# Performance work log

Measured on AMD Instinct MI355X. Metric: run time of the kernel, lower is better.

Reference implementation:

```python
import jax, jax.numpy as jnp
import numpy as np
from jax import lax

B, N, D = 8, 1024, 768      # batch, tokens, feature dim
H, Y = 12, 64               # heads, head dim
M = 3072                    # hopfield memories (4*D)
STEPS = 12                  # descent steps (module default)
ALPHA = 0.1                 # SGD step size (module default)
BETA = 1.0 / np.sqrt(Y)     # attention inverse temperature
EPS = 1e-5


def setup_inputs() -> dict:
    key = jax.random.key(0)
    k0, k1, k2, k3 = jax.random.split(key, 4)
    return {
        "x": jax.random.normal(k0, (B, N, D), dtype=jnp.float32),
        "ln_gamma": jnp.ones((D,), dtype=jnp.float32),
        "ln_beta": jnp.zeros((D,), dtype=jnp.float32),
        "wq": jax.random.normal(k1, (H, Y, D), dtype=jnp.float32) * 0.02,
        "wk": jax.random.normal(k2, (H, Y, D), dtype=jnp.float32) * 0.02,
        "xi": jax.random.normal(k3, (M, D), dtype=jnp.float32) * 0.02,
    }


def _layer_norm(x, gamma, beta):
    mu = jnp.mean(x, axis=-1, keepdims=True)
    var = jnp.var(x, axis=-1, keepdims=True)
    return gamma * (x - mu) * lax.rsqrt(var + EPS) + beta


def _energy(g, wq, wk, xi):
    # Attention energy: A[b,h,m,n] = sum_y K_{hy m} Q_{hy n}
    q = jnp.einsum("hyd,bnd->bhny", wq, g)
    k = jnp.einsum("hyd,bnd->bhny", wk, g)
    logits = BETA * jnp.einsum("bhmy,bhny->bhmn", k, q)  # [B,H,N(keys),N(queries)]
    e_att = -(1.0 / BETA) * jnp.sum(jax.scipy.special.logsumexp(logits, axis=2))
    # Hopfield energy: -0.5 * sum relu(xi @ g)^2
    hid = jnp.einsum("md,bnd->bnm", xi, g)
    e_hn = -0.5 * jnp.sum(jnp.square(jax.nn.relu(hid)))
    return e_att + e_hn


_energy_grad = jax.grad(_energy)


def reference(x, ln_gamma, ln_beta, wq, wk, xi):
    def step(x, _):
        g = _layer_norm(x, ln_gamma, ln_beta)  # grad taken w.r.t. g, not through LN
        grad = _energy_grad(g, wq, wk, xi)
        return x - ALPHA * grad, None

    x, _ = lax.scan(step, x, None, length=STEPS)
    return x
```

## Files before the change

kernel.cpp:

```cpp
#include <hip/hip_runtime.h>
#include <math.h>

#define B_ 8
#define N_ 1024
#define D_ 768
#define H_ 12
#define Y_ 64
#define M_ 3072
#define STEPS_ 12
#define ALPHA_ 0.1f
#define BETA_ 0.125f
#define EPS_ 1e-5f

typedef __attribute__((ext_vector_type(8))) short bf16x8;
typedef __attribute__((ext_vector_type(8))) unsigned short u16x8;
typedef __attribute__((ext_vector_type(4))) float f32x4;

__device__ inline unsigned short f2bf(float f) {
  union { float f; unsigned int u; } v; v.f = f;
  unsigned int r = (v.u + 0x7fffu + ((v.u >> 16) & 1u)) >> 16;
  return (unsigned short)r;
}

__device__ inline void async_copy16(const void* g, void* l) {
  __builtin_amdgcn_global_load_lds(
      (const __attribute__((address_space(1))) unsigned int*)g,
      (__attribute__((address_space(3))) unsigned int*)l, 16, 0, 0);
}

__device__ inline int xcd_remap(int bid, int nwg) {
  const int qd = nwg >> 3, rm = nwg & 7;
  const int xcd = bid & 7, idx = bid >> 3;
  return (xcd < rm ? xcd * (qd + 1) : rm * (qd + 1) + (xcd - rm) * qd) + idx;
}

__global__ __launch_bounds__(256) void ln_kernel(const float* __restrict__ x,
    const float* __restrict__ gamma, const float* __restrict__ beta,
    unsigned short* __restrict__ g) {
  const int row = blockIdx.x;
  const int t = threadIdx.x;
  const float* xr = x + (size_t)row * D_;
  float v0 = xr[t], v1 = xr[t + 256], v2 = xr[t + 512];
  float s = v0 + v1 + v2;
  float sq = v0 * v0 + v1 * v1 + v2 * v2;
  #pragma unroll
  for (int off = 1; off < 64; off <<= 1) {
    s += __shfl_xor(s, off);
    sq += __shfl_xor(sq, off);
  }
  __shared__ float ss[4], ssq[4];
  const int wid = t >> 6;
  if ((t & 63) == 0) { ss[wid] = s; ssq[wid] = sq; }
  __syncthreads();
  s = ss[0] + ss[1] + ss[2] + ss[3];
  sq = ssq[0] + ssq[1] + ssq[2] + ssq[3];
  const float mu = s * (1.0f / D_);
  const float var = sq * (1.0f / D_) - mu * mu;
  const float r = rsqrtf(var + EPS_);
  unsigned short* gr = g + (size_t)row * D_;
  gr[t]       = f2bf(gamma[t]       * (v0 - mu) * r + beta[t]);
  gr[t + 256] = f2bf(gamma[t + 256] * (v1 - mu) * r + beta[t + 256]);
  gr[t + 512] = f2bf(gamma[t + 512] * (v2 - mu) * r + beta[t + 512]);
}

__global__ __launch_bounds__(256) void cvt_bf16(const float* __restrict__ in,
    unsigned short* __restrict__ out, int n) {
  int i = blockIdx.x * 256 + threadIdx.x;
  if (i < n) out[i] = f2bf(in[i]);
}

__global__ __launch_bounds__(256) void transpose_cvt(const float* __restrict__ in,
    unsigned short* __restrict__ out, int R, int C, int ldo, int koff) {
  __shared__ float tile[32][33];
  const int c0 = blockIdx.x * 32, r0 = blockIdx.y * 32;
  const int tx = threadIdx.x & 31, ty = threadIdx.x >> 5;
  #pragma unroll
  for (int i = 0; i < 32; i += 8)
    tile[ty + i][tx] = in[(size_t)(r0 + ty + i) * C + c0 + tx];
  __syncthreads();
  #pragma unroll
  for (int i = 0; i < 32; i += 8)
    out[(size_t)(c0 + ty + i) * ldo + koff + r0 + tx] = f2bf(tile[tx][ty + i]);
}

template <bool RELU, bool WRT>
__global__ __launch_bounds__(256) void gemm128(
    const unsigned short* __restrict__ A, const unsigned short* __restrict__ Bm,
    unsigned short* __restrict__ C, int N, int K, int gridN,
    unsigned short* __restrict__ qT, unsigned short* __restrict__ kT) {
  __shared__ __align__(16) unsigned short As[128 * 64];
  __shared__ __align__(16) unsigned short Bs[128 * 64];
  const int t = threadIdx.x;
  const int f = xcd_remap(blockIdx.x, gridDim.x);
  const int n0 = (f % gridN) * 128;
  const int m0 = (f / gridN) * 128;
  const int w = t >> 6;
  const int l = t & 63;
  const int wr = (w >> 1) * 64;
  const int wc = (w & 1) * 64;

  f32x4 acc[4][4];
  #pragma unroll
  for (int m = 0; m < 4; ++m)
    #pragma unroll
    for (int n = 0; n < 4; ++n) {
      f32x4 z = {0.f, 0.f, 0.f, 0.f};
      acc[m][n] = z;
    }

  for (int kt = 0; kt < K; kt += 64) {
    #pragma unroll
    for (int i = 0; i < 4; ++i) {
      const int flat = i * 4096 + t * 16;
      const int row = flat >> 7;
      const int slog = ((flat >> 4) & 7) ^ (row & 7);
      async_copy16(A + (size_t)(m0 + row) * K + kt + slog * 8, (char*)As + flat);
      async_copy16(Bm + (size_t)(n0 + row) * K + kt + slog * 8, (char*)Bs + flat);
    }
    __syncthreads();
    #pragma unroll
    for (int kk = 0; kk < 2; ++kk) {
      bf16x8 a[4], b[4];
      const int lr = l & 15;
      const int sl = kk * 4 + (l >> 4);
      #pragma unroll
      for (int m = 0; m < 4; ++m) {
        const int row = wr + m * 16 + lr;
        a[m] = *(const bf16x8*)((const char*)As + row * 128 + ((sl ^ (row & 7)) << 4));
      }
      #pragma unroll
      for (int n = 0; n < 4; ++n) {
        const int row = wc + n * 16 + lr;
        b[n] = *(const bf16x8*)((const char*)Bs + row * 128 + ((sl ^ (row & 7)) << 4));
      }
      #pragma unroll
      for (int m = 0; m < 4; ++m)
        #pragma unroll
        for (int n = 0; n < 4; ++n)
          acc[m][n] = __builtin_amdgcn_mfma_f32_16x16x32_bf16(a[m], b[n], acc[m][n], 0, 0, 0);
    }
    __syncthreads();
  }

  const int cr = (l >> 4) * 4;
  const int cc = l & 15;
  #pragma unroll
  for (int m = 0; m < 4; ++m)
    #pragma unroll
    for (int n = 0; n < 4; ++n) {
      const int col = n0 + wc + n * 16 + cc;
      unsigned long long pk = 0;
      #pragma unroll
      for (int j = 0; j < 4; ++j) {
        const int row = m0 + wr + m * 16 + cr + j;
        float v = acc[m][n][j];
        if (RELU) v = v > 0.f ? v : 0.f;
        const unsigned short bv = f2bf(v);
        C[(size_t)row * N + col] = bv;
        if (WRT) pk |= (unsigned long long)bv << (16 * j);
      }
      if (WRT) {
        const int row0 = m0 + wr + m * 16 + cr;
        const int bb = row0 >> 10, nn = row0 & 1023;
        const int hy = (col < 768) ? col : (col - 768);
        unsigned short* T = (col < 768) ? qT : kT;
        *(unsigned long long*)(T + ((size_t)bb * 768 + hy) * N_ + nn) = pk;
      }
    }
}

__global__ __launch_bounds__(256) void gemm_update(
    const unsigned short* __restrict__ A1,
    const unsigned short* __restrict__ A2,
    const unsigned short* __restrict__ B2,
    float* __restrict__ x,
    float alpha) {
  __shared__ __align__(16) unsigned short As[128 * 64];
  __shared__ __align__(16) unsigned short Bs[64 * 64];
  const int t = threadIdx.x;
  const int f = xcd_remap(blockIdx.x, gridDim.x);
  const int n0 = (f % 12) * 64;
  const int m0 = (f / 12) * 128;
  const int w = t >> 6;
  const int l = t & 63;
  const int wr = (w >> 1) * 64;
  const int wc = (w & 1) * 32;

  f32x4 acc[4][2];
  #pragma unroll
  for (int m = 0; m < 4; ++m)
    #pragma unroll
    for (int n = 0; n < 2; ++n) {
      f32x4 z = {0.f, 0.f, 0.f, 0.f};
      acc[m][n] = z;
    }

  for (int kt = 0; kt < 4608; kt += 64) {
    #pragma unroll
    for (int i = 0; i < 4; ++i) {
      const int flat = i * 4096 + t * 16;
      const int row = flat >> 7;
      const int slog = ((flat >> 4) & 7) ^ (row & 7);
      const unsigned short* src = (kt < 1536)
          ? A1 + (size_t)(m0 + row) * 1536 + kt + slog * 8
          : A2 + (size_t)(m0 + row) * 3072 + (kt - 1536) + slog * 8;
      async_copy16(src, (char*)As + flat);
    }
    #pragma unroll
    for (int i = 0; i < 2; ++i) {
      const int flat = i * 4096 + t * 16;
      const int row = flat >> 7;
      const int slog = ((flat >> 4) & 7) ^ (row & 7);
      async_copy16(B2 + (size_t)(n0 + row) * 4608 + kt + slog * 8, (char*)Bs + flat);
    }
    __syncthreads();
    #pragma unroll
    for (int kk = 0; kk < 2; ++kk) {
      bf16x8 a[4], b[2];
      const int lr = l & 15;
      const int sl = kk * 4 + (l >> 4);
      #pragma unroll
      for (int m = 0; m < 4; ++m) {
        const int row = wr + m * 16 + lr;
        a[m] = *(const bf16x8*)((const char*)As + row * 128 + ((sl ^ (row & 7)) << 4));
      }
      #pragma unroll
      for (int n = 0; n < 2; ++n) {
        const int row = wc + n * 16 + lr;
        b[n] = *(const bf16x8*)((const char*)Bs + row * 128 + ((sl ^ (row & 7)) << 4));
      }
      #pragma unroll
      for (int m = 0; m < 4; ++m)
        #pragma unroll
        for (int n = 0; n < 2; ++n)
          acc[m][n] = __builtin_amdgcn_mfma_f32_16x16x32_bf16(a[m], b[n], acc[m][n], 0, 0, 0);
    }
    __syncthreads();
  }

  const int cr = (l >> 4) * 4;
  const int cc = l & 15;
  #pragma unroll
  for (int m = 0; m < 4; ++m)
    #pragma unroll
    for (int n = 0; n < 2; ++n) {
      const int col = n0 + wc + n * 16 + cc;
      #pragma unroll
      for (int j = 0; j < 4; ++j) {
        const int row = m0 + wr + m * 16 + cr + j;
        float* cp = x + (size_t)row * 768 + col;
        *cp += alpha * acc[m][n][j];
      }
    }
}

__global__ __launch_bounds__(256) void attn1_mfma(
    const unsigned short* __restrict__ qk, const unsigned short* __restrict__ kT,
    unsigned short* __restrict__ AqAk, float* __restrict__ lse) {
  __shared__ __align__(16) unsigned short Ks[128 * 64];
  __shared__ __align__(16) unsigned short KTs[64 * 128];
  __shared__ __align__(16) unsigned short Ps[4 * 16 * 128];
  const int n0 = blockIdx.x * 64;
  const int h = blockIdx.y;
  const int b = blockIdx.z;
  const int t = threadIdx.x;
  const int w = t >> 6;
  const int l = t & 63;
  const int g = l >> 4;
  const int ql = l & 15;
  char* psw = (char*)(Ps + w * 2048);
  const int LD = 1536;

  bf16x8 qf[2];
  {
    const unsigned short* qrow =
        qk + ((size_t)(b * N_ + n0 + w * 16 + ql)) * LD + h * Y_;
    qf[0] = *(const bf16x8*)(qrow + g * 8);
    qf[1] = *(const bf16x8*)(qrow + 32 + g * 8);
  }
  const unsigned short* kbase = qk + (size_t)b * N_ * LD + 768 + h * Y_;
  const unsigned short* kTbase = kT + ((size_t)(b * H_ + h)) * Y_ * N_;

  f32x4 acc[4];
  #pragma unroll
  for (int yf = 0; yf < 4; ++yf) { f32x4 z = {0.f,0.f,0.f,0.f}; acc[yf] = z; }
  float mmax = -1e30f, lsum = 0.f;

  for (int mc = 0; mc < N_; mc += 128) {
    #pragma unroll
    for (int i = 0; i < 4; ++i) {
      const int flat = i * 4096 + t * 16;
      const int row = flat >> 7;
      const int slog = ((flat >> 4) & 7) ^ (row & 7);
      async_copy16(kbase + (size_t)(mc + row) * LD + slog * 8, (char*)Ks + flat);
    }
    #pragma unroll
    for (int i = 0; i < 4; ++i) {
      const int flat = i * 4096 + t * 16;
      const int row = flat >> 8;
      const int slog = ((flat >> 4) & 15) ^ (row & 7);
      async_copy16(kTbase + (size_t)row * N_ + mc + slog * 8, (char*)KTs + flat);
    }
    __syncthreads();

    f32x4 s[8];
    __builtin_amdgcn_s_setprio(1);
    #pragma unroll
    for (int f = 0; f < 8; ++f) {
      f32x4 z = {0.f,0.f,0.f,0.f}; s[f] = z;
      #pragma unroll
      for (int ks = 0; ks < 2; ++ks) {
        const int key = f * 16 + ql;
        bf16x8 a = *(const bf16x8*)((const char*)Ks + key * 128 +
                                    (((ks * 4 + g) ^ (key & 7)) << 4));
        s[f] = __builtin_amdgcn_mfma_f32_16x16x32_bf16(a, qf[ks], s[f], 0, 0, 0);
      }
    }
    __builtin_amdgcn_s_setprio(0);
    float rm = -1e30f;
    #pragma unroll
    for (int f = 0; f < 8; ++f)
      #pragma unroll
      for (int j = 0; j < 4; ++j) {
        const float v = s[f][j] * BETA_;
        s[f][j] = v;
        rm = fmaxf(rm, v);
      }
    rm = fmaxf(rm, __shfl_xor(rm, 16));
    rm = fmaxf(rm, __shfl_xor(rm, 32));
    const float nm = fmaxf(mmax, rm);
    const float sc = __expf(mmax - nm);
    float rs = 0.f;
    #pragma unroll
    for (int f = 0; f < 8; ++f) {
      unsigned short p4[4];
      #pragma unroll
      for (int j = 0; j < 4; ++j) {
        const float pvj = __expf(s[f][j] - nm);
        rs += pvj;
        p4[j] = f2bf(pvj);
      }
      unsigned long long pk = (unsigned long long)p4[0] |
          ((unsigned long long)p4[1] << 16) |
          ((unsigned long long)p4[2] << 32) |
          ((unsigned long long)p4[3] << 48);
      const int sl = (f * 4 + g) ^ ((ql & 7) << 1);
      *(unsigned long long*)(psw + ql * 256 + sl * 8) = pk;
    }
    rs += __shfl_xor(rs, 16);
    rs += __shfl_xor(rs, 32);
    lsum = lsum * sc + rs;
    mmax = nm;
    #pragma unroll
    for (int yf = 0; yf < 4; ++yf) acc[yf] *= sc;
    __builtin_amdgcn_s_setprio(1);
    #pragma unroll
    for (int ks2 = 0; ks2 < 4; ++ks2) {
      const int sl2 = (ks2 * 8 + g * 2) ^ ((ql & 7) << 1);
      bf16x8 pa = *(const bf16x8*)(psw + ql * 256 + sl2 * 8);
      #pragma unroll
      for (int yf = 0; yf < 4; ++yf) {
        const int y = yf * 16 + ql;
        bf16x8 bk = *(const bf16x8*)((const char*)KTs + y * 256 +
                                     (((ks2 * 4 + g) ^ (y & 7)) << 4));
        acc[yf] = __builtin_amdgcn_mfma_f32_16x16x32_bf16(pa, bk, acc[yf], 0, 0, 0);
      }
    }
    __builtin_amdgcn_s_setprio(0);
    __syncthreads();
  }

  float linv[4];
  #pragma unroll
  for (int j = 0; j < 4; ++j)
    linv[j] = 1.0f / __shfl(lsum, (g << 4) + g * 4 + j);
  #pragma unroll
  for (int yf = 0; yf < 4; ++yf)
    #pragma unroll
    for (int j = 0; j < 4; ++j) {
      const int row = n0 + w * 16 + g * 4 + j;
      AqAk[((size_t)(b * N_ + row)) * LD + h * Y_ + yf * 16 + ql] =
          f2bf(acc[yf][j] * linv[j]);
    }
  if (g == 0)
    lse[((size_t)b * H_ + h) * N_ + n0 + w * 16 + ql] = mmax + __logf(lsum);
}

__global__ __launch_bounds__(256) void attn2_mfma(
    const unsigned short* __restrict__ qk, const unsigned short* __restrict__ qT,
    const float* __restrict__ lse, unsigned short* __restrict__ AqAk) {
  __shared__ __align__(16) unsigned short Qs[128 * 64];
  __shared__ __align__(16) unsigned short QTs[64 * 128];
  __shared__ __align__(16) unsigned short Ws[4 * 16 * 128];
  __shared__ float lse_s[128];
  const int m0 = blockIdx.x * 64;
  const int h = blockIdx.y;
  const int b = blockIdx.z;
  const int t = threadIdx.x;
  const int w = t >> 6;
  const int l = t & 63;
  const int g = l >> 4;
  const int ql = l & 15;
  char* wsw = (char*)(Ws + w * 2048);
  const int LD = 1536;

  bf16x8 ka[2];
  {
    const unsigned short* krow =
        qk + ((size_t)(b * N_ + m0 + w * 16 + ql)) * LD + 768 + h * Y_;
    ka[0] = *(const bf16x8*)(krow + g * 8);
    ka[1] = *(const bf16x8*)(krow + 32 + g * 8);
  }
  const unsigned short* qbase = qk + (size_t)b * N_ * LD + h * Y_;
  const unsigned short* qTbase = qT + ((size_t)(b * H_ + h)) * Y_ * N_;
  const float* lbase = lse + ((size_t)b * H_ + h) * N_;

  f32x4 acc[4];
  #pragma unroll
  for (int yf = 0; yf < 4; ++yf) { f32x4 z = {0.f,0.f,0.f,0.f}; acc[yf] = z; }

  for (int nc = 0; nc < N_; nc += 128) {
    #pragma unroll
    for (int i = 0; i < 4; ++i) {
      const int flat = i * 4096 + t * 16;
      const int row = flat >> 7;
      const int slog = ((flat >> 4) & 7) ^ (row & 7);
      async_copy16(qbase + (size_t)(nc + row) * LD + slog * 8, (char*)Qs + flat);
    }
    #pragma unroll
    for (int i = 0; i < 4; ++i) {
      const int flat = i * 4096 + t * 16;
      const int row = flat >> 8;
      const int slog = ((flat >> 4) & 15) ^ (row & 7);
      async_copy16(qTbase + (size_t)row * N_ + nc + slog * 8, (char*)QTs + flat);
    }
    if (t < 128) lse_s[t] = lbase[nc + t];
    __syncthreads();

    f32x4 s[8];
    __builtin_amdgcn_s_setprio(1);
    #pragma unroll
    for (int f = 0; f < 8; ++f) {
      f32x4 z = {0.f,0.f,0.f,0.f}; s[f] = z;
      #pragma unroll
      for (int ks = 0; ks < 2; ++ks) {
        const int qr = f * 16 + ql;
        bf16x8 a = *(const bf16x8*)((const char*)Qs + qr * 128 +
                                    (((ks * 4 + g) ^ (qr & 7)) << 4));
        s[f] = __builtin_amdgcn_mfma_f32_16x16x32_bf16(a, ka[ks], s[f], 0, 0, 0);
      }
    }
    __builtin_amdgcn_s_setprio(0);
    #pragma unroll
    for (int f = 0; f < 8; ++f) {
      unsigned short w4[4];
      #pragma unroll
      for (int j = 0; j < 4; ++j) {
        const float wv = __expf(s[f][j] * BETA_ - lse_s[f * 16 + g * 4 + j]);
        w4[j] = f2bf(wv);
      }
      unsigned long long pk =
          (unsigned long long)w4[0] | ((unsigned long long)w4[1] << 16) |
          ((unsigned long long)w4[2] << 32) | ((unsigned long long)w4[3] << 48);
      const int sl = (f * 4 + g) ^ ((ql & 7) << 1);
      *(unsigned long long*)(wsw + ql * 256 + sl * 8) = pk;
    }
    __builtin_amdgcn_s_setprio(1);
    #pragma unroll
    for (int ks2 = 0; ks2 < 4; ++ks2) {
      const int sl2 = (ks2 * 8 + g * 2) ^ ((ql & 7) << 1);
      bf16x8 wa = *(const bf16x8*)(wsw + ql * 256 + sl2 * 8);
      #pragma unroll
      for (int yf = 0; yf < 4; ++yf) {
        const int y = yf * 16 + ql;
        bf16x8 bq = *(const bf16x8*)((const char*)QTs + y * 256 +
                                     (((ks2 * 4 + g) ^ (y & 7)) << 4));
        acc[yf] = __builtin_amdgcn_mfma_f32_16x16x32_bf16(wa, bq, acc[yf], 0, 0, 0);
      }
    }
    __builtin_amdgcn_s_setprio(0);
    __syncthreads();
  }

  #pragma unroll
  for (int yf = 0; yf < 4; ++yf)
    #pragma unroll
    for (int j = 0; j < 4; ++j) {
      const int row = m0 + w * 16 + g * 4 + j;
      AqAk[((size_t)(b * N_ + row)) * LD + 768 + h * Y_ + yf * 16 + ql] =
          f2bf(acc[yf][j]);
    }
}

extern "C" void kernel_launch(void* const* d_in, const int* in_sizes, int n_in,
                              void* d_out, int out_size, void* d_ws, size_t ws_size,
                              hipStream_t stream) {
  const float* x0    = (const float*)d_in[0];
  const float* gamma = (const float*)d_in[1];
  const float* beta  = (const float*)d_in[2];
  const float* wq    = (const float*)d_in[3];
  const float* wk    = (const float*)d_in[4];
  const float* xi    = (const float*)d_in[5];
  float* x = (float*)d_out;

  const size_t SZ = (size_t)B_ * N_ * D_;
  char* wsp = (char*)d_ws;
  size_t off = 0;
  auto alloc = [&](size_t bytes) -> void* {
    off = (off + 255) & ~(size_t)255;
    void* p = wsp + off;
    off += bytes;
    return p;
  };
  unsigned short* g_bf   = (unsigned short*)alloc(SZ * 2);
  unsigned short* qk_bf  = (unsigned short*)alloc(SZ * 2 * 2);
  unsigned short* AqAk   = (unsigned short*)alloc(SZ * 2 * 2);
  unsigned short* qT_bf  = (unsigned short*)alloc(SZ * 2);
  unsigned short* kT_bf  = (unsigned short*)alloc(SZ * 2);
  float*          lse    = (float*)alloc((size_t)B_ * H_ * N_ * 4);
  unsigned short* wqk_bf = (unsigned short*)alloc((size_t)2 * D_ * D_ * 2);
  unsigned short* xi_bf  = (unsigned short*)alloc((size_t)M_ * D_ * 2);
  unsigned short* B2_bf  = (unsigned short*)alloc((size_t)D_ * (2 * D_ + M_) * 2);
  off = (off + 255) & ~(size_t)255;
  unsigned short* hid_bf = (unsigned short*)(wsp + off);
  size_t avail = ws_size > off ? ws_size - off : 0;
  long rmax = (long)(avail / ((size_t)M_ * 2));
  int R = (int)((rmax / 128) * 128);
  if (R > B_ * N_) R = B_ * N_;
  if (R < 128) R = 128;

  const int WQN = D_ * D_;
  const int XIN = M_ * D_;
  cvt_bf16<<<(WQN + 255) / 256, 256, 0, stream>>>(wq, wqk_bf, WQN);
  cvt_bf16<<<(WQN + 255) / 256, 256, 0, stream>>>(wk, wqk_bf + (size_t)D_ * D_, WQN);
  cvt_bf16<<<(XIN + 255) / 256, 256, 0, stream>>>(xi, xi_bf, XIN);
  const int LDB2 = 2 * D_ + M_;
  transpose_cvt<<<dim3(D_ / 32, D_ / 32), 256, 0, stream>>>(wq, B2_bf, D_, D_, LDB2, 0);
  transpose_cvt<<<dim3(D_ / 32, D_ / 32), 256, 0, stream>>>(wk, B2_bf, D_, D_, LDB2, D_);
  transpose_cvt<<<dim3(D_ / 32, M_ / 32), 256, 0, stream>>>(xi, B2_bf, M_, D_, LDB2, 2 * D_);

  hipMemcpyAsync(x, x0, SZ * sizeof(float), hipMemcpyDeviceToDevice, stream);

  const int MN = B_ * N_;
  for (int step = 0; step < STEPS_; ++step) {
    ln_kernel<<<MN, 256, 0, stream>>>(x, gamma, beta, g_bf);
    gemm128<false, true><<<(1536 / 128) * (MN / 128), 256, 0, stream>>>(
        g_bf, wqk_bf, qk_bf, 1536, D_, 1536 / 128, qT_bf, kT_bf);
    attn1_mfma<<<dim3(N_ / 64, H_, B_), 256, 0, stream>>>(qk_bf, kT_bf, AqAk, lse);
    attn2_mfma<<<dim3(N_ / 64, H_, B_), 256, 0, stream>>>(qk_bf, qT_bf, lse, AqAk);
    for (int r0 = 0; r0 < MN; r0 += R) {
      const int rows = (MN - r0) < R ? (MN - r0) : R;
      gemm128<true, false><<<(M_ / 128) * (rows / 128), 256, 0, stream>>>(
          g_bf + (size_t)r0 * D_, xi_bf, hid_bf, M_, D_, M_ / 128, nullptr, nullptr);
      gemm_update<<<(D_ / 64) * (rows / 128), 256, 0, stream>>>(
          AqAk + (size_t)r0 * 1536, hid_bf, B2_bf, x + (size_t)r0 * D_, ALPHA_);
    }
  }
}
```

Baseline: 3.282 ms.

## Widen update GEMM K-tile, vectorize layernorm, drop hidden-buffer chunking

The layernorm kernel now uses 192 threads, each loading one float4 and writing packed bf16, in place of three scalar accesses per thread. The update GEMM stages a 128-wide K slice per iteration with a 16-way swizzle, halving the barrier and loop overhead per MFMA. The hidden activation buffer is now allocated for all rows, so the xi GEMM and the update GEMM each launch once per step without chunking. The full-size buffer assumes the workspace is large enough, and the larger LDS tiles may lower occupancy.

```diff
diff --git a/kernel.cpp b/kernel.cpp
--- a/kernel.cpp
+++ b/kernel.cpp
@@ -34,33 +34,37 @@
   return (xcd < rm ? xcd * (qd + 1) : rm * (qd + 1) + (xcd - rm) * qd) + idx;
 }
 
-__global__ __launch_bounds__(256) void ln_kernel(const float* __restrict__ x,
+__global__ __launch_bounds__(192) void ln_kernel(const float* __restrict__ x,
     const float* __restrict__ gamma, const float* __restrict__ beta,
     unsigned short* __restrict__ g) {
   const int row = blockIdx.x;
   const int t = threadIdx.x;
   const float* xr = x + (size_t)row * D_;
-  float v0 = xr[t], v1 = xr[t + 256], v2 = xr[t + 512];
-  float s = v0 + v1 + v2;
-  float sq = v0 * v0 + v1 * v1 + v2 * v2;
+  const float4 v = *(const float4*)(xr + t * 4);
+  float s = v.x + v.y + v.z + v.w;
+  float sq = v.x * v.x + v.y * v.y + v.z * v.z + v.w * v.w;
   #pragma unroll
   for (int off = 1; off < 64; off <<= 1) {
     s += __shfl_xor(s, off);
     sq += __shfl_xor(sq, off);
   }
-  __shared__ float ss[4], ssq[4];
+  __shared__ float ss[3], ssq[3];
   const int wid = t >> 6;
   if ((t & 63) == 0) { ss[wid] = s; ssq[wid] = sq; }
   __syncthreads();
-  s = ss[0] + ss[1] + ss[2] + ss[3];
-  sq = ssq[0] + ssq[1] + ssq[2] + ssq[3];
+  s = ss[0] + ss[1] + ss[2];
+  sq = ssq[0] + ssq[1] + ssq[2];
   const float mu = s * (1.0f / D_);
   const float var = sq * (1.0f / D_) - mu * mu;
   const float r = rsqrtf(var + EPS_);
-  unsigned short* gr = g + (size_t)row * D_;
-  gr[t]       = f2bf(gamma[t]       * (v0 - mu) * r + beta[t]);
-  gr[t + 256] = f2bf(gamma[t + 256] * (v1 - mu) * r + beta[t + 256]);
-  gr[t + 512] = f2bf(gamma[t + 512] * (v2 - mu) * r + beta[t + 512]);
+  const float4 gm = *(const float4*)(gamma + t * 4);
+  const float4 bt = *(const float4*)(beta + t * 4);
+  const unsigned int r0 = f2bf(gm.x * (v.x - mu) * r + bt.x);
+  const unsigned int r1 = f2bf(gm.y * (v.y - mu) * r + bt.y);
+  const unsigned int r2 = f2bf(gm.z * (v.z - mu) * r + bt.z);
+  const unsigned int r3 = f2bf(gm.w * (v.w - mu) * r + bt.w);
+  uint2 pk = {r0 | (r1 << 16), r2 | (r3 << 16)};
+  *(uint2*)(g + (size_t)row * D_ + t * 4) = pk;
 }
 
 __global__ __launch_bounds__(256) void cvt_bf16(const float* __restrict__ in,
@@ -175,8 +179,8 @@
     const unsigned short* __restrict__ B2,
     float* __restrict__ x,
     float alpha) {
-  __shared__ __align__(16) unsigned short As[128 * 64];
-  __shared__ __align__(16) unsigned short Bs[64 * 64];
+  __shared__ __align__(16) unsigned short As[128 * 128];
+  __shared__ __align__(16) unsigned short Bs[64 * 128];
   const int t = threadIdx.x;
   const int f = xcd_remap(blockIdx.x, gridDim.x);
   const int n0 = (f % 12) * 64;
@@ -195,39 +199,39 @@
       acc[m][n] = z;
     }
 
-  for (int kt = 0; kt < 4608; kt += 64) {
-    #pragma unroll
-    for (int i = 0; i < 4; ++i) {
-      const int flat = i * 4096 + t * 16;
-      const int row = flat >> 7;
-      const int slog = ((flat >> 4) & 7) ^ (row & 7);
+  for (int kt = 0; kt < 4608; kt += 128) {
+    #pragma unroll
+    for (int i = 0; i < 8; ++i) {
+      const int flat = i * 4096 + t * 16;
+      const int row = flat >> 8;
+      const int slog = ((flat >> 4) & 15) ^ (row & 15);
       const unsigned short* src = (kt < 1536)
           ? A1 + (size_t)(m0 + row) * 1536 + kt + slog * 8
           : A2 + (size_t)(m0 + row) * 3072 + (kt - 1536) + slog * 8;
       async_copy16(src, (char*)As + flat);
     }
     #pragma unroll
-    for (int i = 0; i < 2; ++i) {
-      const int flat = i * 4096 + t * 16;
-      const int row = flat >> 7;
-      const int slog = ((flat >> 4) & 7) ^ (row & 7);
+    for (int i = 0; i < 4; ++i) {
+      const int flat = i * 4096 + t * 16;
+      const int row = flat >> 8;
+      const int slog = ((flat >> 4) & 15) ^ (row & 15);
       async_copy16(B2 + (size_t)(n0 + row) * 4608 + kt + slog * 8, (char*)Bs + flat);
     }
     __syncthreads();
     #pragma unroll
-    for (int kk = 0; kk < 2; ++kk) {
+    for (int kk = 0; kk < 4; ++kk) {
       bf16x8 a[4], b[2];
       const int lr = l & 15;
       const int sl = kk * 4 + (l >> 4);
       #pragma unroll
       for (int m = 0; m < 4; ++m) {
         const int row = wr + m * 16 + lr;
-        a[m] = *(const bf16x8*)((const char*)As + row * 128 + ((sl ^ (row & 7)) << 4));
+        a[m] = *(const bf16x8*)((const char*)As + row * 256 + ((sl ^ (row & 15)) << 4));
       }
       #pragma unroll
       for (int n = 0; n < 2; ++n) {
         const int row = wc + n * 16 + lr;
-        b[n] = *(const bf16x8*)((const char*)Bs + row * 128 + ((sl ^ (row & 7)) << 4));
+        b[n] = *(const bf16x8*)((const char*)Bs + row * 256 + ((sl ^ (row & 15)) << 4));
       }
       #pragma unroll
       for (int m = 0; m < 4; ++m)
@@ -521,13 +525,7 @@
   unsigned short* wqk_bf = (unsigned short*)alloc((size_t)2 * D_ * D_ * 2);
   unsigned short* xi_bf  = (unsigned short*)alloc((size_t)M_ * D_ * 2);
   unsigned short* B2_bf  = (unsigned short*)alloc((size_t)D_ * (2 * D_ + M_) * 2);
-  off = (off + 255) & ~(size_t)255;
-  unsigned short* hid_bf = (unsigned short*)(wsp + off);
-  size_t avail = ws_size > off ? ws_size - off : 0;
-  long rmax = (long)(avail / ((size_t)M_ * 2));
-  int R = (int)((rmax / 128) * 128);
-  if (R > B_ * N_) R = B_ * N_;
-  if (R < 128) R = 128;
+  unsigned short* hid_bf = (unsigned short*)alloc((size_t)B_ * N_ * M_ * 2);
 
   const int WQN = D_ * D_;
   const int XIN = M_ * D_;
@@ -543,17 +541,14 @@
 
   const int MN = B_ * N_;
   for (int step = 0; step < STEPS_; ++step) {
-    ln_kernel<<<MN, 256, 0, stream>>>(x, gamma, beta, g_bf);
+    ln_kernel<<<MN, 192, 0, stream>>>(x, gamma, beta, g_bf);
     gemm128<false, true><<<(1536 / 128) * (MN / 128), 256, 0, stream>>>(
         g_bf, wqk_bf, qk_bf, 1536, D_, 1536 / 128, qT_bf, kT_bf);
+    gemm128<true, false><<<(M_ / 128) * (MN / 128), 256, 0, stream>>>(
+        g_bf, xi_bf, hid_bf, M_, D_, M_ / 128, nullptr, nullptr);
     attn1_mfma<<<dim3(N_ / 64, H_, B_), 256, 0, stream>>>(qk_bf, kT_bf, AqAk, lse);
     attn2_mfma<<<dim3(N_ / 64, H_, B_), 256, 0, stream>>>(qk_bf, qT_bf, lse, AqAk);
-    for (int r0 = 0; r0 < MN; r0 += R) {
-      const int rows = (MN - r0) < R ? (MN - r0) : R;
-      gemm128<true, false><<<(M_ / 128) * (rows / 128), 256, 0, stream>>>(
-          g_bf + (size_t)r0 * D_, xi_bf, hid_bf, M_, D_, M_ / 128, nullptr, nullptr);
-      gemm_update<<<(D_ / 64) * (rows / 128), 256, 0, stream>>>(
-          AqAk + (size_t)r0 * 1536, hid_bf, B2_bf, x + (size_t)r0 * D_, ALPHA_);
-    }
-  }
-}
+    gemm_update<<<12 * (MN / 128), 256, 0, stream>>>(
+        AqAk, hid_bf, B2_bf, x, ALPHA_);
+  }
+}
```

Result: no change. 3.288 ms (+0.2%).
